# Kernel optimization log

Measured on AMD Instinct MI355X. Metric: run time of the kernel, lower is better.

Reference implementation:

```python
import jax, jax.numpy as jnp
import numpy as np

PAD = 1          # kernel offsets lie in [-1, 1] for kernel_size=3
COORD_MAX = 128  # coordinates quantized to [0, 128)
S = COORD_MAX + 2 * PAD  # per-dimension encoding stride (130)


def setup_inputs() -> dict:
    key = jax.random.key(0)
    B, N, D = 4, 50000, 3
    coordinates = jax.random.randint(
        jax.random.fold_in(key, 0), (B, N, D), 0, COORD_MAX, dtype=jnp.int32)
    # batch_indices[b, n] == b, matching how the torch code partitions rows
    batch_indices = jnp.broadcast_to(jnp.arange(B, dtype=jnp.int32)[:, None], (B, N))
    # 3^3 hypercube kernel offsets, lexicographic order (KernelGenerator semantics)
    r = jnp.arange(-1, 2, dtype=jnp.int32)
    kernel_offsets = jnp.stack(jnp.meshgrid(r, r, r, indexing='ij'), axis=-1).reshape(-1, 3)
    return {"coordinates": coordinates, "batch_indices": batch_indices,
            "kernel_offsets": kernel_offsets}


def reference(coordinates, batch_indices, kernel_offsets):
    """Vectorized equivalent of LocalSelfAttention.compute_kernel_mapping.

    Returns (input_idx, output_idx, rel_pos_idx, output_key_tensor, num_unique).
    The first three are [B, N, K] (the torch kernel_map flattened row-major is
    exactly zip of these), output_key_tensor is [L, D] padded with -1 beyond
    num_unique rows, with unique keys in first-occurrence (insertion) order --
    identical to the Python dict-hashing loop.
    """
    B, N, D = coordinates.shape
    K = kernel_offsets.shape[0]
    L = B * N * K

    # neighbor coords per (point, offset): [B, N, K, D]
    nb = coordinates[:, :, None, :] + kernel_offsets[None, None, :, :]

    # encode (batch_id, neighbor_coord) into a single int32 key
    enc = jnp.broadcast_to(batch_indices[:, :, None], (B, N, K)).astype(jnp.int32)
    for d in range(D):
        enc = enc * S + (nb[..., d] + PAD)  # max ~ 4*130^3 < 2^31
    keys = enc.reshape(L)

    # sort-based dedup preserving first-occurrence order
    order = jnp.argsort(keys, stable=True)              # [L]
    sk = keys[order]
    new_group = jnp.concatenate([jnp.ones((1,), bool), sk[1:] != sk[:-1]])
    gid_sorted = jnp.cumsum(new_group.astype(jnp.int32)) - 1  # group id per sorted slot
    num_unique = gid_sorted[-1] + 1

    # first flat position where each group's key occurs (empty groups -> int32 max)
    first_occ = jax.ops.segment_min(order, gid_sorted, num_segments=L)
    # insertion-order index of each group (padded groups stably rank last)
    group_rank = jnp.argsort(jnp.argsort(first_occ))

    # scatter group ids back to original flat order, then map to insertion rank
    gid = jnp.zeros((L,), jnp.int32).at[order].set(gid_sorted)
    output_idx = group_rank[gid].reshape(B, N, K).astype(jnp.int32)

    # representative encoded key per group, reordered to insertion order
    rep_key = jax.ops.segment_min(sk, gid_sorted, num_segments=L)
    enc_ord = jnp.zeros((L,), keys.dtype).at[group_rank].set(rep_key)

    # decode neighbor coordinates (drop the batch component, as torch does)
    coords_dec = []
    e = enc_ord
    for _ in range(D):
        coords_dec.append(e % S - PAD)
        e = e // S
    out_coords = jnp.stack(coords_dec[::-1], axis=-1)  # [L, D]
    valid = (jnp.arange(L) < num_unique)[:, None]
    output_key_tensor = jnp.where(valid, out_coords, -1)

    input_idx = jnp.broadcast_to(jnp.arange(N, dtype=jnp.int32)[None, :, None], (B, N, K))
    rel_pos_idx = jnp.broadcast_to(jnp.arange(K, dtype=jnp.int32)[None, None, :], (B, N, K))
    return (input_idx, output_idx, rel_pos_idx, output_key_tensor, num_unique)
```

## Files before the change

### kernel.cpp

```cpp
#include <hip/hip_runtime.h>
#include <cstdint>

#define B_   4
#define N_   50000
#define K_   27
#define P_   (B_ * N_)
#define L_   (P_ * K_)
#define S_   130
#define PL_  (S_ * S_)
#define BB_  (S_ * S_ * S_)
#define KS_  (B_ * BB_)
#define W_   (L_ / 64)
#define NBW  ((W_ + 255) / 256)
#define BIG_ 0x7f000000

__global__ __launch_bounds__(256) void k_init_fill(int* __restrict__ P1,
                                                   int* __restrict__ out0,
                                                   int* __restrict__ out2) {
    int i = blockIdx.x * blockDim.x + threadIdx.x;
    if (i < KS_) P1[i] = BIG_;
    if (i < L_) {
        int p = i / K_;
        int k = i - p * K_;
        out0[i] = p - (p / N_) * N_;
        out2[i] = k;
    }
}

__global__ __launch_bounds__(256) void k_ptab(const int* __restrict__ coords,
                                              const int* __restrict__ bidx,
                                              int* __restrict__ P1) {
    int p = blockIdx.x * blockDim.x + threadIdx.x;
    if (p >= P_) return;
    int b = bidx[p];
    int x = coords[3 * p + 0] + 1;
    int y = coords[3 * p + 1] + 1;
    int z = coords[3 * p + 2] + 1;
    int idx = ((b * S_ + x) * S_ + y) * S_ + z;
    atomicMin(&P1[idx], p << 5);
}

__global__ __launch_bounds__(256) void k_minz(const int* __restrict__ src,
                                              int* __restrict__ dst) {
    int i = blockIdx.x * blockDim.x + threadIdx.x;
    if (i >= KS_) return;
    int z = i % S_;
    int v = src[i] + 1;
    if (z > 0)      v = min(v, src[i - 1] + 2);
    if (z < S_ - 1) v = min(v, src[i + 1]);
    dst[i] = v;
}

__global__ __launch_bounds__(256) void k_miny(const int* __restrict__ src,
                                              int* __restrict__ dst) {
    int i = blockIdx.x * blockDim.x + threadIdx.x;
    if (i >= KS_) return;
    int y = (i / S_) % S_;
    int v = src[i] + 3;
    if (y > 0)      v = min(v, src[i - S_] + 6);
    if (y < S_ - 1) v = min(v, src[i + S_]);
    dst[i] = v;
}

__global__ __launch_bounds__(256) void k_minx(const int* __restrict__ src,
                                              int* __restrict__ dst) {
    int i = blockIdx.x * blockDim.x + threadIdx.x;
    if (i >= KS_) return;
    int x = (i / PL_) % S_;
    int v = src[i] + 9;
    if (x > 0)      v = min(v, src[i - PL_] + 18);
    if (x < S_ - 1) v = min(v, src[i + PL_]);
    dst[i] = v;
}

__global__ __launch_bounds__(256) void k_flag_bitmap(const int* __restrict__ coords,
                                                     const int* __restrict__ bidx,
                                                     const int* __restrict__ koffs,
                                                     const int* __restrict__ M,
                                                     int* __restrict__ mArr,
                                                     unsigned long long* __restrict__ bitmap) {
    int l = blockIdx.x * blockDim.x + threadIdx.x;
    if (l >= L_) return;
    int p = l / K_;
    int k = l - p * K_;
    int b = bidx[p];
    int cx = coords[3 * p + 0] + koffs[3 * k + 0] + 1;
    int cy = coords[3 * p + 1] + koffs[3 * k + 1] + 1;
    int cz = coords[3 * p + 2] + koffs[3 * k + 2] + 1;
    int idx = ((b * S_ + cx) * S_ + cy) * S_ + cz;
    int m32 = M[idx];
    mArr[l] = m32;
    unsigned long long bal = __ballot(m32 == ((p << 5) | k));
    if ((threadIdx.x & 63) == 0) bitmap[l >> 6] = bal;
}

__global__ __launch_bounds__(256) void k_scan_words(const unsigned long long* __restrict__ bitmap,
                                                    int* __restrict__ wpre,
                                                    int* __restrict__ bsum) {
    __shared__ int sh[256];
    int w = blockIdx.x * 256 + threadIdx.x;
    int c = (w < W_) ? __popcll(bitmap[w]) : 0;
    sh[threadIdx.x] = c;
    __syncthreads();
    for (int off = 1; off < 256; off <<= 1) {
        int t = (threadIdx.x >= off) ? sh[threadIdx.x - off] : 0;
        __syncthreads();
        sh[threadIdx.x] += t;
        __syncthreads();
    }
    if (w < W_) wpre[w] = sh[threadIdx.x] - c;
    if (threadIdx.x == 255) bsum[blockIdx.x] = sh[255];
}

__global__ __launch_bounds__(512) void k_scan_block(int* __restrict__ bsum,
                                                    int* __restrict__ num_unique_out) {
    __shared__ int sh[512];
    int i = threadIdx.x;
    int v = (i < NBW) ? bsum[i] : 0;
    sh[i] = v;
    __syncthreads();
    for (int off = 1; off < 512; off <<= 1) {
        int t = (i >= off) ? sh[i - off] : 0;
        __syncthreads();
        sh[i] += t;
        __syncthreads();
    }
    if (i < NBW) bsum[i] = sh[i] - v;
    if (i == 0) num_unique_out[0] = sh[511];
}

__global__ __launch_bounds__(256) void k_finalize(const int* __restrict__ coords,
                                                  const int* __restrict__ koffs,
                                                  const unsigned long long* __restrict__ bitmap,
                                                  const int* __restrict__ wpre,
                                                  const int* __restrict__ bsum,
                                                  const int* __restrict__ numuniq,
                                                  int* __restrict__ out1,
                                                  int* __restrict__ outkey) {
    int l = blockIdx.x * blockDim.x + threadIdx.x;
    if (l >= L_) return;
    int m32 = out1[l];
    int m = (m32 >> 5) * K_ + (m32 & 31);
    int w = m >> 6;
    unsigned long long word = bitmap[w];
    unsigned long long mask = (1ull << (m & 63)) - 1ull;
    int rank = wpre[w] + bsum[w >> 8] + (int)__popcll(word & mask);
    if (m == l) {
        int p = l / K_;
        int k = l - p * K_;
        outkey[3 * rank + 0] = coords[3 * p + 0] + koffs[3 * k + 0];
        outkey[3 * rank + 1] = coords[3 * p + 1] + koffs[3 * k + 1];
        outkey[3 * rank + 2] = coords[3 * p + 2] + koffs[3 * k + 2];
    }
    out1[l] = rank;
    if (l >= numuniq[0]) {
        outkey[3 * l + 0] = -1;
        outkey[3 * l + 1] = -1;
        outkey[3 * l + 2] = -1;
    }
}

extern "C" void kernel_launch(void* const* d_in, const int* in_sizes, int n_in,
                              void* d_out, int out_size, void* d_ws, size_t ws_size,
                              hipStream_t stream) {
    const int* coords = (const int*)d_in[0];
    const int* bidx   = (const int*)d_in[1];
    const int* koffs  = (const int*)d_in[2];

    int* out      = (int*)d_out;
    int* out0     = out;
    int* out1     = out + L_;
    int* out2     = out + 2 * L_;
    int* outkey   = out + 3 * L_;
    int* numuniq  = out + 6 * L_;

    int* P1 = (int*)d_ws;
    unsigned long long* bitmap = (unsigned long long*)(P1 + KS_);
    int* wpre = (int*)(bitmap + W_);
    int* bsum = wpre + W_;

    int* A = outkey;

    k_init_fill   <<<(KS_ + 255) / 256, 256, 0, stream>>>(P1, out0, out2);
    k_ptab        <<<(P_ + 255) / 256, 256, 0, stream>>>(coords, bidx, P1);
    k_minz        <<<(KS_ + 255) / 256, 256, 0, stream>>>(P1, A);
    k_miny        <<<(KS_ + 255) / 256, 256, 0, stream>>>(A, P1);
    k_minx        <<<(KS_ + 255) / 256, 256, 0, stream>>>(P1, A);
    k_flag_bitmap <<<(L_ + 255) / 256, 256, 0, stream>>>(coords, bidx, koffs, A, out1, bitmap);
    k_scan_words  <<<NBW, 256, 0, stream>>>(bitmap, wpre, bsum);
    k_scan_block  <<<1, 512, 0, stream>>>(bsum, numuniq);
    k_finalize    <<<(L_ + 255) / 256, 256, 0, stream>>>(coords, koffs, bitmap, wpre, bsum,
                                                         numuniq, out1, outkey);
}
```

Baseline: 162.6 us.

## Fuse z/y min passes in LDS, memset init, fold index fills into flag kernel

Merges the separate z and y stencil passes into one kernel that stages a whole y-z plane in shared memory, removing one full global read/write sweep of the dense coordinate table. The init kernel is replaced by a byte memset to 0x7f7f7f7f as the sentinel. The input_idx and rel_pos_idx fills move into the flag/bitmap kernel, so no separate pass writes them. The fused kernel uses about 135KB of LDS per block, which limits it to one 256-thread block per CU and may reduce latency hiding.

```diff
diff --git a/kernel.cpp b/kernel.cpp
--- a/kernel.cpp
+++ b/kernel.cpp
@@ -8,24 +8,9 @@
 #define L_   (P_ * K_)
 #define S_   130
 #define PL_  (S_ * S_)
-#define BB_  (S_ * S_ * S_)
-#define KS_  (B_ * BB_)
+#define KS_  (B_ * S_ * S_ * S_)
 #define W_   (L_ / 64)
 #define NBW  ((W_ + 255) / 256)
-#define BIG_ 0x7f000000
-
-__global__ __launch_bounds__(256) void k_init_fill(int* __restrict__ P1,
-                                                   int* __restrict__ out0,
-                                                   int* __restrict__ out2) {
-    int i = blockIdx.x * blockDim.x + threadIdx.x;
-    if (i < KS_) P1[i] = BIG_;
-    if (i < L_) {
-        int p = i / K_;
-        int k = i - p * K_;
-        out0[i] = p - (p / N_) * N_;
-        out2[i] = k;
-    }
-}
 
 __global__ __launch_bounds__(256) void k_ptab(const int* __restrict__ coords,
                                               const int* __restrict__ bidx,
@@ -40,30 +25,33 @@
     atomicMin(&P1[idx], p << 5);
 }
 
-__global__ __launch_bounds__(256) void k_minz(const int* __restrict__ src,
-                                              int* __restrict__ dst) {
-    int i = blockIdx.x * blockDim.x + threadIdx.x;
-    if (i >= KS_) return;
-    int z = i % S_;
-    int v = src[i] + 1;
-    if (z > 0)      v = min(v, src[i - 1] + 2);
-    if (z < S_ - 1) v = min(v, src[i + 1]);
-    dst[i] = v;
+__global__ __launch_bounds__(256) void k_zy(const int* __restrict__ src,
+                                            int* __restrict__ dst) {
+    __shared__ int pl[PL_];
+    __shared__ int tz[PL_];
+    const int* s = src + (size_t)blockIdx.x * PL_;
+    int* d       = dst + (size_t)blockIdx.x * PL_;
+    for (int i = threadIdx.x; i < PL_; i += 256) pl[i] = s[i];
+    __syncthreads();
+    for (int i = threadIdx.x; i < PL_; i += 256) {
+        int z = i % S_;
+        int v = pl[i] + 1;
+        if (z > 0)      v = min(v, pl[i - 1] + 2);
+        if (z < S_ - 1) v = min(v, pl[i + 1]);
+        tz[i] = v;
+    }
+    __syncthreads();
+    for (int i = threadIdx.x; i < PL_; i += 256) {
+        int y = i / S_;
+        int v = tz[i] + 3;
+        if (y > 0)      v = min(v, tz[i - S_] + 6);
+        if (y < S_ - 1) v = min(v, tz[i + S_]);
+        d[i] = v;
+    }
 }
 
-__global__ __launch_bounds__(256) void k_miny(const int* __restrict__ src,
-                                              int* __restrict__ dst) {
-    int i = blockIdx.x * blockDim.x + threadIdx.x;
-    if (i >= KS_) return;
-    int y = (i / S_) % S_;
-    int v = src[i] + 3;
-    if (y > 0)      v = min(v, src[i - S_] + 6);
-    if (y < S_ - 1) v = min(v, src[i + S_]);
-    dst[i] = v;
-}
-
-__global__ __launch_bounds__(256) void k_minx(const int* __restrict__ src,
-                                              int* __restrict__ dst) {
+__global__ __launch_bounds__(256) void k_x(const int* __restrict__ src,
+                                           int* __restrict__ dst) {
     int i = blockIdx.x * blockDim.x + threadIdx.x;
     if (i >= KS_) return;
     int x = (i / PL_) % S_;
@@ -78,11 +66,15 @@
                                                      const int* __restrict__ koffs,
                                                      const int* __restrict__ M,
                                                      int* __restrict__ mArr,
-                                                     unsigned long long* __restrict__ bitmap) {
+                                                     unsigned long long* __restrict__ bitmap,
+                                                     int* __restrict__ out0,
+                                                     int* __restrict__ out2) {
     int l = blockIdx.x * blockDim.x + threadIdx.x;
     if (l >= L_) return;
     int p = l / K_;
     int k = l - p * K_;
+    out0[l] = p - (p / N_) * N_;
+    out2[l] = k;
     int b = bidx[p];
     int cx = coords[3 * p + 0] + koffs[3 * k + 0] + 1;
     int cy = coords[3 * p + 1] + koffs[3 * k + 1] + 1;
@@ -181,12 +173,12 @@
 
     int* A = outkey;
 
-    k_init_fill   <<<(KS_ + 255) / 256, 256, 0, stream>>>(P1, out0, out2);
+    hipMemsetAsync(P1, 0x7f, (size_t)KS_ * sizeof(int), stream);
     k_ptab        <<<(P_ + 255) / 256, 256, 0, stream>>>(coords, bidx, P1);
-    k_minz        <<<(KS_ + 255) / 256, 256, 0, stream>>>(P1, A);
-    k_miny        <<<(KS_ + 255) / 256, 256, 0, stream>>>(A, P1);
-    k_minx        <<<(KS_ + 255) / 256, 256, 0, stream>>>(P1, A);
-    k_flag_bitmap <<<(L_ + 255) / 256, 256, 0, stream>>>(coords, bidx, koffs, A, out1, bitmap);
+    k_zy          <<<B_ * S_, 256, 0, stream>>>(P1, A);
+    k_x           <<<(KS_ + 255) / 256, 256, 0, stream>>>(A, P1);
+    k_flag_bitmap <<<(L_ + 255) / 256, 256, 0, stream>>>(coords, bidx, koffs, P1, out1, bitmap,
+                                                         out0, out2);
     k_scan_words  <<<NBW, 256, 0, stream>>>(bitmap, wpre, bsum);
     k_scan_block  <<<1, 512, 0, stream>>>(bsum, numuniq);
     k_finalize    <<<(L_ + 255) / 256, 256, 0, stream>>>(coords, koffs, bitmap, wpre, bsum,
```

Result: slower. 171.2 us (+5.3%).
